# Kernel tuning notes

Hardware: AMD Instinct MI355X
Metric: run time of the kernel (lower is better)

## Reference

```python
import jax, jax.numpy as jnp
import numpy as np
from jax import lax

FACTOR = 2
GAIN = 1.0
RESAMPLE = (1.0, 3.0, 3.0, 1.0)


def _setup_fir():
    k = np.asarray(RESAMPLE, dtype=np.float32)
    k = np.outer(k, k)
    k /= k.sum()
    return k * (GAIN * FACTOR ** 2)  # 4x4, scaled by factor^2 for upsampling


def setup_inputs() -> dict:
    key = jax.random.key(0)
    k1, k2, k3 = jax.random.split(key, 3)
    x = jax.random.normal(k1, (16, 256, 64, 64), jnp.float32)
    weight = jax.random.normal(k2, (256, 256, 3, 3), jnp.float32) * 0.05
    bias = jax.random.normal(k3, (256,), jnp.float32) * 0.05
    return {"x": x, "weight": weight, "bias": bias}


def _upsample_conv_2d(x, w):
    # Equivalent to torch: conv_transpose2d(x, flip(w).transpose(0,1), stride=FACTOR)
    # The pre-flip cancels conv_transpose's kernel flip, so this is an
    # input-dilated cross-correlation with the original OIHW weight.
    outC, inC, kh, kw = w.shape
    y = lax.conv_general_dilated(
        x, w, window_strides=(1, 1),
        padding=[(kh - 1, kh - 1), (kw - 1, kw - 1)],
        lhs_dilation=(FACTOR, FACTOR),
        dimension_numbers=('NCHW', 'OIHW', 'NCHW'))  # (N, outC, (H-1)*f+kh, (W-1)*f+kw)

    # upfirdn2d(y, fir, up=1, down=1, pad=((p+1)//2 + factor-1, p//2 + 1))
    fir = jnp.asarray(_setup_fir())
    fh, fw = fir.shape
    p = fh - FACTOR - (kw - 1)  # = 0 for k=3, factor=2, 4-tap FIR
    pad0 = (p + 1) // 2 + FACTOR - 1  # = 1
    pad1 = p // 2 + 1                  # = 1
    # upfirdn2d_native correlates with the flipped FIR, depthwise per channel
    dw = jnp.broadcast_to(fir[::-1, ::-1], (outC, 1, fh, fw))
    out = lax.conv_general_dilated(
        y, dw, window_strides=(1, 1),
        padding=[(pad0, pad1), (pad0, pad1)],
        feature_group_count=outC,
        dimension_numbers=('NCHW', 'OIHW', 'NCHW'))  # (N, outC, H*f, W*f)
    return out


def reference(x, weight, bias):
    out = _upsample_conv_2d(x, weight)
    return out + bias.reshape(1, -1, 1, 1)
```

## Files before the change

kernel.cpp:

```cpp
#include <hip/hip_runtime.h>
#include <hip/hip_bf16.h>

using bf16 = __hip_bfloat16;
typedef __bf16 bf16x8 __attribute__((ext_vector_type(8)));
typedef float f32x4 __attribute__((ext_vector_type(4)));
typedef short short8 __attribute__((ext_vector_type(8)));
typedef _Float16 h2 __attribute__((ext_vector_type(2)));

#define AS1(p) ((const __attribute__((address_space(1))) void*)(p))
#define AS3(p) ((__attribute__((address_space(3))) void*)(p))

#define YSTRIDE 4368

__global__ void prep_wt_k(const float* __restrict__ w, bf16* __restrict__ wt) {
  const int o = blockIdx.x, i = threadIdx.x;
  const float* wp = w + (size_t)(o * 256 + i) * 9;
#pragma unroll
  for (int p = 0; p < 9; ++p)
    wt[(size_t)p * 65536 + o * 256 + i] = __float2bfloat16(wp[p]);
}

__global__ void zring_k(bf16* __restrict__ xpad) {
  const int bid = blockIdx.x;
  const int n = bid / 33, cg = bid - n * 33;
  const int t = threadIdx.x;
  const int cell = cg * 8 + (t >> 5);
  if (cell >= 260) return;
  int row, col;
  if (cell < 66) { row = 0; col = cell; }
  else if (cell < 132) { row = 65; col = cell - 66; }
  else if (cell < 196) { row = cell - 131; col = 0; }
  else { row = cell - 195; col = 65; }
  const int ch = (t & 31) * 8;
  short8 z = {0, 0, 0, 0, 0, 0, 0, 0};
  *(short8*)(xpad + (((size_t)n * 66 + row) * 66 + col) * 256 + ch) = z;
}

__global__ void xpose_k(const float* __restrict__ x, bf16* __restrict__ xpad) {
  const int b = blockIdx.x;
  const int icb = b & 3, iy = (b >> 2) & 63, n = b >> 8;
  __shared__ bf16 lds[64][72];
  const int t = threadIdx.x;
  const int c = t >> 2, ixq = t & 3;
  const float* src = x + (((size_t)(n * 256 + icb * 64 + c) * 64 + iy) * 64);
#pragma unroll
  for (int rep = 0; rep < 4; ++rep) {
    const int ix0 = ixq * 16 + rep * 4;
    float4 v = *reinterpret_cast<const float4*>(src + ix0);
    lds[ix0 + 0][c] = __float2bfloat16(v.x);
    lds[ix0 + 1][c] = __float2bfloat16(v.y);
    lds[ix0 + 2][c] = __float2bfloat16(v.z);
    lds[ix0 + 3][c] = __float2bfloat16(v.w);
  }
  __syncthreads();
  const int ix = t >> 2, cseg = (t & 3) * 16;
  bf16* dst = xpad + (((size_t)(n * 66 + iy + 1) * 66 + ix + 1) * 256 + icb * 64 + cseg);
  *reinterpret_cast<short8*>(dst) = *reinterpret_cast<const short8*>(&lds[ix][cseg]);
  *reinterpret_cast<short8*>(dst + 8) = *reinterpret_cast<const short8*>(&lds[ix][cseg + 8]);
}

__device__ __forceinline__ int xcdswz(int b, int n) {
  const int q = n >> 3, r = n & 7;
  const int xcd = b & 7, idx = b >> 3;
  return (xcd < r ? xcd * (q + 1) : r * (q + 1) + (xcd - r) * q) + idx;
}

template <int PLANE>
__device__ __forceinline__ void passA_body(int bid, const bf16* __restrict__ xpad,
                                           const bf16* __restrict__ wt,
                                           _Float16* __restrict__ yy, int nimg,
                                           bf16* ldsW, bf16* ldsX) {
  constexpr int M = (PLANE == 0) ? 4225 : (PLANE == 3) ? 4096 : 4160;
  constexpr int T = (M + 255) >> 8;
  constexpr int NT = (PLANE == 0) ? 4 : (PLANE == 3) ? 1 : 2;
  constexpr int NSTEP = NT * 4;
  constexpr int AOFF = (PLANE >= 2) ? 1 : 0;
  constexpr int BOFF = (PLANE & 1) ? 1 : 0;
  constexpr int DW = (PLANE == 0 || PLANE == 2) ? 65 : 64;
  constexpr int TAPI_all[4][4] = {{0, 2, 6, 8}, {1, 7, 0, 0}, {3, 5, 0, 0}, {4, 0, 0, 0}};
  constexpr int TDY_all[4][4] = {{0, 0, 1, 1}, {0, 1, 0, 0}, {0, 0, 0, 0}, {0, 0, 0, 0}};
  constexpr int TDX_all[4][4] = {{0, 1, 0, 1}, {0, 0, 0, 0}, {0, 1, 0, 0}, {0, 0, 0, 0}};
  constexpr int MAXS = TDY_all[PLANE][NT - 1] * DW + TDX_all[PLANE][NT - 1];
  constexpr int UR = 256 + MAXS;
  constexpr int XBUF = 328 * 64;

  const int t = threadIdx.x;
  const int tile = bid % T;
  const int nl = bid / T;
  const int m0 = tile * 256;
  const bf16* xn = xpad + (size_t)nl * (66 * 66 * 256);
  _Float16* yn = yy + ((size_t)(PLANE * nimg + nl) * 256) * YSTRIDE;

  const int w = t >> 6, lane = t & 63;
  const int wr = w >> 1, wc = w & 1;
  const int lr = lane & 15, lg = lane >> 4;

  auto dec = [](int m, int& a, int& b) {
    if (PLANE == 0 || PLANE == 2) { a = m / 65; b = m - a * 65; }
    else { a = m >> 6; b = m & 63; }
  };

  int wOffB[4];
#pragma unroll
  for (int r = 0; r < 4; ++r) {
    const int idx = r * 512 + t;
    const int row = idx >> 3;
    wOffB[r] = (row * 256) * 2 + (((idx & 7) * 16) ^ ((row & 7) << 4));
  }

  int xOffU[6];
  const int nxc = (UR * 8 - t + 511) >> 9;
#pragma unroll
  for (int k = 0; k < 6; ++k) {
    const int cidx = k * 512 + t;
    if (cidx < UR * 8) {
      const int row = cidx >> 3;
      const int swz = ((cidx & 7) * 16) ^ ((row & 7) << 4);
      const int ms = m0 + row;
      if (ms < M) {
        int a, b;
        dec(ms, a, b);
        xOffU[k] = (((a + AOFF) * 66 + (b + BOFF)) * 256) * 2 + swz;
      } else {
        xOffU[k] = (65 * 66 * 256) * 2 + swz;
      }
    }
  }

  auto stage_w = [&](int step, int buf) {
    const int tap = step % NT, icb = step / NT;
    const int wtoff = (TAPI_all[PLANE][tap] * 65536 + icb * 64) * 2;
    bf16* lw = ldsW + (size_t)buf * (256 * 64);
#pragma unroll
    for (int r = 0; r < 4; ++r)
      __builtin_amdgcn_global_load_lds(AS1((const char*)wt + wOffB[r] + wtoff),
                                       AS3(lw + (size_t)(r * 512 + (t & 448)) * 8), 16, 0, 0);
  };

  auto stage_x = [&](int icb, int buf) {
    const int xtoffB = icb * 128;
    bf16* lx = ldsX + (size_t)buf * XBUF;
    for (int k = 0; k < nxc; ++k) {
      const int cidx = k * 512 + t;
      __builtin_amdgcn_global_load_lds(AS1((const char*)xn + xOffU[k] + xtoffB),
                                       AS3(lx + (size_t)(cidx & ~63) * 8), 16, 0, 0);
    }
  };

  f32x4 acc[4][8];
#pragma unroll
  for (int i = 0; i < 4; ++i)
#pragma unroll
    for (int j = 0; j < 8; ++j) acc[i][j] = (f32x4){0.f, 0.f, 0.f, 0.f};

  stage_w(0, 0);
  stage_x(0, 0);
  __syncthreads();

  for (int step = 0; step < NSTEP; ++step) {
    const int icb = step / NT, tap = step - icb * NT;
    const int next = step + 1;
    if (next < NSTEP) {
      stage_w(next, next & 1);
      if (next - (next / NT) * NT == 0) stage_x(next / NT, (next / NT) & 1);
    }
    const int sOff = TDY_all[PLANE][tap] * DW + TDX_all[PLANE][tap];
    const bf16* lw = ldsW + (size_t)(step & 1) * (256 * 64);
    const bf16* lx = ldsX + (size_t)(icb & 1) * XBUF;
#pragma unroll
    for (int kk = 0; kk < 2; ++kk) {
      bf16x8 af[4], bfr[8];
#pragma unroll
      for (int i = 0; i < 4; ++i) {
        const int row = wr * 64 + i * 16 + lr;
        const int off = row * 128 + ((kk * 64 + lg * 16) ^ ((row & 7) << 4));
        af[i] = *(const bf16x8*)((const char*)lw + off);
      }
#pragma unroll
      for (int j = 0; j < 8; ++j) {
        const int row = wc * 128 + j * 16 + lr + sOff;
        const int off = row * 128 + ((kk * 64 + lg * 16) ^ ((row & 7) << 4));
        bfr[j] = *(const bf16x8*)((const char*)lx + off);
      }
#pragma unroll
      for (int i = 0; i < 4; ++i)
#pragma unroll
        for (int j = 0; j < 8; ++j)
          acc[i][j] = __builtin_amdgcn_mfma_f32_16x16x32_bf16(af[i], bfr[j], acc[i][j], 0, 0, 0);
    }
    __syncthreads();
  }

#pragma unroll
  for (int i = 0; i < 4; ++i) {
    const int ocb = wr * 64 + i * 16 + lg * 4;
#pragma unroll
    for (int j = 0; j < 8; ++j) {
      const int m = m0 + wc * 128 + j * 16 + lr;
      if (m < M) {
        int a, b;
        dec(m, a, b);
        const size_t sp = (size_t)(a + 1) * 66 + (b + 1);
#pragma unroll
        for (int reg = 0; reg < 4; ++reg)
          yn[(size_t)(ocb + reg) * YSTRIDE + sp] = (_Float16)acc[i][j][reg];
      }
    }
  }
}

__global__ __launch_bounds__(512) void passA_all(const bf16* __restrict__ xpad,
                                                 const bf16* __restrict__ wt,
                                                 _Float16* __restrict__ yy, int nimg) {
  __shared__ __attribute__((aligned(16))) bf16 ldsW[2][256 * 64];
  __shared__ __attribute__((aligned(16))) bf16 ldsX[2][328 * 64];
  int bid = blockIdx.x;
  const int S0 = nimg * 17, S1 = nimg * 17, S2 = nimg * 17;
  if (bid < S0) { passA_body<0>(xcdswz(bid, S0), xpad, wt, yy, nimg, &ldsW[0][0], &ldsX[0][0]); return; }
  bid -= S0;
  if (bid < S1) { passA_body<1>(xcdswz(bid, S1), xpad, wt, yy, nimg, &ldsW[0][0], &ldsX[0][0]); return; }
  bid -= S1;
  if (bid < S2) { passA_body<2>(xcdswz(bid, S2), xpad, wt, yy, nimg, &ldsW[0][0], &ldsX[0][0]); return; }
  bid -= S2;
  passA_body<3>(xcdswz(bid, nimg * 16), xpad, wt, yy, nimg, &ldsW[0][0], &ldsX[0][0]);
}

#define BSTRIDE 2248

__global__ void passB_k(const _Float16* __restrict__ yy, const float* __restrict__ bias,
                        float* __restrict__ out, int nimg, int n0) {
  __shared__ _Float16 ldsY[4][BSTRIDE];
  const int b = blockIdx.x;
  const int h = b & 1, c = (b >> 1) & 255, nl = b >> 9;
  const int R0 = h * 32;
  const int t = threadIdx.x;
  const size_t PS = (size_t)nimg * 256 * YSTRIDE;
  const _Float16* base = yy + ((size_t)nl * 256 + c) * YSTRIDE;

  for (int idx = t; idx < 4 * 281; idx += 256) {
    const int pl = idx / 281, off = idx - pl * 281;
    *(float4*)(&ldsY[pl][off * 8]) =
        *(const float4*)((const char*)(base + (size_t)pl * PS) + R0 * 132 + (size_t)off * 16);
  }
  __syncthreads();
  const int brel = h ? 33 : 0;
  for (int idx = t; idx < 268; idx += 256) {
    if (idx < 68) {
      const int r = idx >> 1, col = (idx & 1) * 65;
      ldsY[1][r * 66 + col] = (_Float16)0.f;
    } else if (idx < 134) {
      ldsY[2][brel * 66 + (idx - 68)] = (_Float16)0.f;
    } else if (idx < 200) {
      ldsY[3][brel * 66 + (idx - 134)] = (_Float16)0.f;
    } else {
      const int k = idx - 200;
      const int r = k >> 1, col = (k & 1) * 65;
      ldsY[3][r * 66 + col] = (_Float16)0.f;
    }
  }
  __syncthreads();

  const int q = t & 31, g = t >> 5;
  const float bv = bias[c];
  float* ob = out + ((size_t)(n0 + nl) * 256 + c) * 16384;
  const int r0 = g * 4;

  float eeA[4], eeB[4], oeA[4], oeB[4], oeC[4];
  float eoA[4], eoB[4], ooA[4], ooB[4], ooC[4];

#define LD4(dst, pl, row)                                          \
  { const h2 u0 = *(const h2*)(&ldsY[pl][(row) * 66 + 2 * q]);     \
    const h2 u1 = *(const h2*)(&ldsY[pl][(row) * 66 + 2 * q + 2]); \
    dst[0] = (float)u0[0]; dst[1] = (float)u0[1];                  \
    dst[2] = (float)u1[0]; dst[3] = (float)u1[1]; }

  LD4(eeA, 0, r0 + 1); LD4(eeB, 0, r0 + 2);
  LD4(oeA, 2, r0);     LD4(oeB, 2, r0 + 1); LD4(oeC, 2, r0 + 2);
  LD4(eoA, 1, r0 + 1); LD4(eoB, 1, r0 + 2);
  LD4(ooA, 3, r0);     LD4(ooB, 3, r0 + 1); LD4(ooC, 3, r0 + 2);

#pragma unroll
  for (int oi = 0; oi < 4; ++oi) {
    const int o = R0 + r0 + oi;
    float rceq[2][3], rcoq[2][4];
#pragma unroll
    for (int k = 0; k < 3; ++k) {
      const int vi = k + 1;
      rceq[0][k] = 0.75f * eeA[vi] + 0.25f * eeB[vi] + 0.25f * oeA[vi] + 0.75f * oeB[vi];
      rceq[1][k] = 0.25f * eeA[vi] + 0.75f * eeB[vi] + 0.75f * oeB[vi] + 0.25f * oeC[vi];
    }
#pragma unroll
    for (int k = 0; k < 4; ++k) {
      rcoq[0][k] = 0.75f * eoA[k] + 0.25f * eoB[k] + 0.25f * ooA[k] + 0.75f * ooB[k];
      rcoq[1][k] = 0.25f * eoA[k] + 0.75f * eoB[k] + 0.75f * ooB[k] + 0.25f * ooC[k];
    }
#pragma unroll
    for (int py = 0; py < 2; ++py) {
      float4 st;
      st.x = 0.75f * rceq[py][0] + 0.25f * rceq[py][1] + 0.25f * rcoq[py][0] +
             0.75f * rcoq[py][1] + bv;
      st.y = 0.25f * rceq[py][0] + 0.75f * rceq[py][1] + 0.75f * rcoq[py][1] +
             0.25f * rcoq[py][2] + bv;
      st.z = 0.75f * rceq[py][1] + 0.25f * rceq[py][2] + 0.25f * rcoq[py][1] +
             0.75f * rcoq[py][2] + bv;
      st.w = 0.25f * rceq[py][1] + 0.75f * rceq[py][2] + 0.75f * rcoq[py][2] +
             0.25f * rcoq[py][3] + bv;
      *(float4*)(ob + ((size_t)(2 * o + py)) * 128 + 4 * q) = st;
    }
    if (oi < 3) {
#pragma unroll
      for (int k = 0; k < 4; ++k) {
        eeA[k] = eeB[k]; oeA[k] = oeB[k]; oeB[k] = oeC[k];
        eoA[k] = eoB[k]; ooA[k] = ooB[k]; ooB[k] = ooC[k];
      }
      LD4(eeB, 0, r0 + oi + 3);
      LD4(oeC, 2, r0 + oi + 3);
      LD4(eoB, 1, r0 + oi + 3);
      LD4(ooC, 3, r0 + oi + 3);
    }
  }
#undef LD4
}

extern "C" void kernel_launch(void* const* d_in, const int* in_sizes, int n_in,
                              void* d_out, int out_size, void* d_ws, size_t ws_size,
                              hipStream_t stream) {
  const float* x = (const float*)d_in[0];
  const float* wgt = (const float*)d_in[1];
  const float* bias = (const float*)d_in[2];
  float* out = (float*)d_out;

  const size_t XPL = (size_t)66 * 66 * 256;
  const size_t YPN = (size_t)4 * 256 * YSTRIDE;
  const size_t WT_BYTES = (size_t)9 * 256 * 256 * 2;
  int c = 0;
  const int cands[5] = {16, 8, 4, 2, 1};
  for (int ci = 0; ci < 5; ++ci)
    if (WT_BYTES + (size_t)cands[ci] * (XPL + YPN) * 2 <= ws_size) { c = cands[ci]; break; }
  if (c == 0) return;

  bf16* wt = (bf16*)d_ws;
  bf16* xpad = (bf16*)((char*)d_ws + WT_BYTES);
  _Float16* yy = (_Float16*)((char*)d_ws + WT_BYTES + (size_t)c * XPL * 2);

  prep_wt_k<<<256, 256, 0, stream>>>(wgt, wt);

  for (int k = 0; k < 16 / c; ++k) {
    zring_k<<<c * 33, 256, 0, stream>>>(xpad);
    xpose_k<<<c * 256, 256, 0, stream>>>(x + (size_t)k * c * 1048576, xpad);
    passA_all<<<c * 67, 512, 0, stream>>>(xpad, wt, yy, c);
    passB_k<<<c * 512, 256, 0, stream>>>(yy, bias, out, c, k * c);
  }
}
```

Baseline: 233.8 us.

## Split passA output channels into two 128-wide blocks and drop LDS double buffering

Each passA block now computes 128 output channels instead of 256, doubling the grid, halving the accumulator registers per thread, and shrinking the weight tile in LDS. The double-buffered prefetch is replaced by single buffers loaded at the top of each step followed by a barrier. This cuts LDS and register use so more blocks can run per CU and more blocks fill the GPU. The cost is that the x tile is loaded twice (once per channel half) and global loads no longer overlap with MFMA work inside a block.

```diff
diff --git a/kernel.cpp b/kernel.cpp
--- a/kernel.cpp
+++ b/kernel.cpp
@@ -82,17 +82,19 @@
   constexpr int TDX_all[4][4] = {{0, 1, 0, 1}, {0, 0, 0, 0}, {0, 1, 0, 0}, {0, 0, 0, 0}};
   constexpr int MAXS = TDY_all[PLANE][NT - 1] * DW + TDX_all[PLANE][NT - 1];
   constexpr int UR = 256 + MAXS;
-  constexpr int XBUF = 328 * 64;
 
   const int t = threadIdx.x;
-  const int tile = bid % T;
-  const int nl = bid / T;
+  const int oct = bid & 1;
+  const int tmp = bid >> 1;
+  const int tile = tmp % T;
+  const int nl = tmp / T;
   const int m0 = tile * 256;
+  const int oc0 = oct * 128;
   const bf16* xn = xpad + (size_t)nl * (66 * 66 * 256);
   _Float16* yn = yy + ((size_t)(PLANE * nimg + nl) * 256) * YSTRIDE;
 
   const int w = t >> 6, lane = t & 63;
-  const int wr = w >> 1, wc = w & 1;
+  const int wr = w & 1, wc = w >> 1;
   const int lr = lane & 15, lg = lane >> 4;
 
   auto dec = [](int m, int& a, int& b) {
@@ -100,12 +102,12 @@
     else { a = m >> 6; b = m & 63; }
   };
 
-  int wOffB[4];
-#pragma unroll
-  for (int r = 0; r < 4; ++r) {
+  int wOffB[2];
+#pragma unroll
+  for (int r = 0; r < 2; ++r) {
     const int idx = r * 512 + t;
     const int row = idx >> 3;
-    wOffB[r] = (row * 256) * 2 + (((idx & 7) * 16) ^ ((row & 7) << 4));
+    wOffB[r] = ((oc0 + row) * 256) * 2 + (((idx & 7) * 16) ^ ((row & 7) << 4));
   }
 
   int xOffU[6];
@@ -127,65 +129,56 @@
     }
   }
 
-  auto stage_w = [&](int step, int buf) {
+  auto stage_w = [&](int step) {
     const int tap = step % NT, icb = step / NT;
     const int wtoff = (TAPI_all[PLANE][tap] * 65536 + icb * 64) * 2;
-    bf16* lw = ldsW + (size_t)buf * (256 * 64);
-#pragma unroll
-    for (int r = 0; r < 4; ++r)
+#pragma unroll
+    for (int r = 0; r < 2; ++r)
       __builtin_amdgcn_global_load_lds(AS1((const char*)wt + wOffB[r] + wtoff),
-                                       AS3(lw + (size_t)(r * 512 + (t & 448)) * 8), 16, 0, 0);
+                                       AS3(ldsW + (size_t)(r * 512 + (t & 448)) * 8), 16, 0, 0);
   };
 
-  auto stage_x = [&](int icb, int buf) {
+  auto stage_x = [&](int icb) {
     const int xtoffB = icb * 128;
-    bf16* lx = ldsX + (size_t)buf * XBUF;
     for (int k = 0; k < nxc; ++k) {
       const int cidx = k * 512 + t;
       __builtin_amdgcn_global_load_lds(AS1((const char*)xn + xOffU[k] + xtoffB),
-                                       AS3(lx + (size_t)(cidx & ~63) * 8), 16, 0, 0);
+                                       AS3(ldsX + (size_t)(cidx & ~63) * 8), 16, 0, 0);
     }
   };
 
-  f32x4 acc[4][8];
+  f32x4 acc[4][4];
 #pragma unroll
   for (int i = 0; i < 4; ++i)
 #pragma unroll
-    for (int j = 0; j < 8; ++j) acc[i][j] = (f32x4){0.f, 0.f, 0.f, 0.f};
-
-  stage_w(0, 0);
-  stage_x(0, 0);
-  __syncthreads();
+    for (int j = 0; j < 4; ++j) acc[i][j] = (f32x4){0.f, 0.f, 0.f, 0.f};
 
   for (int step = 0; step < NSTEP; ++step) {
     const int icb = step / NT, tap = step - icb * NT;
-    const int next = step + 1;
-    if (next < NSTEP) {
-      stage_w(next, next & 1);
-      if (next - (next / NT) * NT == 0) stage_x(next / NT, (next / NT) & 1);
-    }
+    stage_w(step);
+    if (tap == 0) stage_x(icb);
+    __syncthreads();
+
     const int sOff = TDY_all[PLANE][tap] * DW + TDX_all[PLANE][tap];
-    const bf16* lw = ldsW + (size_t)(step & 1) * (256 * 64);
-    const bf16* lx = ldsX + (size_t)(icb & 1) * XBUF;
 #pragma unroll
     for (int kk = 0; kk < 2; ++kk) {
-      bf16x8 af[4], bfr[8];
+      bf16x8 af[4], bfr[4];
 #pragma unroll
       for (int i = 0; i < 4; ++i) {
         const int row = wr * 64 + i * 16 + lr;
         const int off = row * 128 + ((kk * 64 + lg * 16) ^ ((row & 7) << 4));
-        af[i] = *(const bf16x8*)((const char*)lw + off);
-      }
-#pragma unroll
-      for (int j = 0; j < 8; ++j) {
-        const int row = wc * 128 + j * 16 + lr + sOff;
+        af[i] = *(const bf16x8*)((const char*)ldsW + off);
+      }
+#pragma unroll
+      for (int j = 0; j < 4; ++j) {
+        const int row = wc * 64 + j * 16 + lr + sOff;
         const int off = row * 128 + ((kk * 64 + lg * 16) ^ ((row & 7) << 4));
-        bfr[j] = *(const bf16x8*)((const char*)lx + off);
+        bfr[j] = *(const bf16x8*)((const char*)ldsX + off);
       }
 #pragma unroll
       for (int i = 0; i < 4; ++i)
 #pragma unroll
-        for (int j = 0; j < 8; ++j)
+        for (int j = 0; j < 4; ++j)
           acc[i][j] = __builtin_amdgcn_mfma_f32_16x16x32_bf16(af[i], bfr[j], acc[i][j], 0, 0, 0);
     }
     __syncthreads();
@@ -193,10 +186,10 @@
 
 #pragma unroll
   for (int i = 0; i < 4; ++i) {
-    const int ocb = wr * 64 + i * 16 + lg * 4;
-#pragma unroll
-    for (int j = 0; j < 8; ++j) {
-      const int m = m0 + wc * 128 + j * 16 + lr;
+    const int ocb = oc0 + wr * 64 + i * 16 + lg * 4;
+#pragma unroll
+    for (int j = 0; j < 4; ++j) {
+      const int m = m0 + wc * 64 + j * 16 + lr;
       if (m < M) {
         int a, b;
         dec(m, a, b);
@@ -212,17 +205,17 @@
 __global__ __launch_bounds__(512) void passA_all(const bf16* __restrict__ xpad,
                                                  const bf16* __restrict__ wt,
                                                  _Float16* __restrict__ yy, int nimg) {
-  __shared__ __attribute__((aligned(16))) bf16 ldsW[2][256 * 64];
-  __shared__ __attribute__((aligned(16))) bf16 ldsX[2][328 * 64];
+  __shared__ __attribute__((aligned(16))) bf16 ldsW[128 * 64];
+  __shared__ __attribute__((aligned(16))) bf16 ldsX[328 * 64];
   int bid = blockIdx.x;
-  const int S0 = nimg * 17, S1 = nimg * 17, S2 = nimg * 17;
-  if (bid < S0) { passA_body<0>(xcdswz(bid, S0), xpad, wt, yy, nimg, &ldsW[0][0], &ldsX[0][0]); return; }
+  const int S0 = nimg * 34, S1 = nimg * 34, S2 = nimg * 34;
+  if (bid < S0) { passA_body<0>(xcdswz(bid, S0), xpad, wt, yy, nimg, ldsW, ldsX); return; }
   bid -= S0;
-  if (bid < S1) { passA_body<1>(xcdswz(bid, S1), xpad, wt, yy, nimg, &ldsW[0][0], &ldsX[0][0]); return; }
+  if (bid < S1) { passA_body<1>(xcdswz(bid, S1), xpad, wt, yy, nimg, ldsW, ldsX); return; }
   bid -= S1;
-  if (bid < S2) { passA_body<2>(xcdswz(bid, S2), xpad, wt, yy, nimg, &ldsW[0][0], &ldsX[0][0]); return; }
+  if (bid < S2) { passA_body<2>(xcdswz(bid, S2), xpad, wt, yy, nimg, ldsW, ldsX); return; }
   bid -= S2;
-  passA_body<3>(xcdswz(bid, nimg * 16), xpad, wt, yy, nimg, &ldsW[0][0], &ldsX[0][0]);
+  passA_body<3>(xcdswz(bid, nimg * 32), xpad, wt, yy, nimg, ldsW, ldsX);
 }
 
 #define BSTRIDE 2248
@@ -348,7 +341,7 @@
   for (int k = 0; k < 16 / c; ++k) {
     zring_k<<<c * 33, 256, 0, stream>>>(xpad);
     xpose_k<<<c * 256, 256, 0, stream>>>(x + (size_t)k * c * 1048576, xpad);
-    passA_all<<<c * 67, 512, 0, stream>>>(xpad, wt, yy, c);
+    passA_all<<<c * 134, 512, 0, stream>>>(xpad, wt, yy, c);
     passB_k<<<c * 512, 256, 0, stream>>>(yy, bias, out, c, k * c);
   }
 }
```

New measurement: 245.2 us. 1.05x slower.
